# Performance work log

Measured on AMD Instinct MI355X. Metric: run time of the kernel, lower is better.

## Reference

```python
import jax, jax.numpy as jnp
import numpy as np

B = 256      # events
N_SV = 64    # secondary vertices per event
N_TRK = 512  # tracks per event
N_PFC = 512  # PF candidates per event
K = 8        # kNN neighbors
H = 32       # hidden dim


def _lin_init(key, fan_in, fan_out):
    k1, k2 = jax.random.split(key)
    lim = 1.0 / np.sqrt(fan_in)
    W = jax.random.uniform(k1, (fan_in, fan_out), minval=-lim, maxval=lim, dtype=jnp.float32)
    b = jax.random.uniform(k2, (fan_out,), minval=-lim, maxval=lim, dtype=jnp.float32)
    return W, b


def setup_inputs() -> dict:
    key = jax.random.key(0)
    ks = jax.random.split(key, 16)
    inp = {
        'x_sv': jax.random.normal(ks[0], (B * N_SV, 14), dtype=jnp.float32),
        'x_trk': jax.random.normal(ks[1], (B * N_TRK, 30), dtype=jnp.float32),
        'x_pfc': jax.random.normal(ks[2], (B * N_PFC, 10), dtype=jnp.float32),
        'batch_sv': jnp.repeat(jnp.arange(B, dtype=jnp.int64), N_SV),
        'batch_trk': jnp.repeat(jnp.arange(B, dtype=jnp.int64), N_TRK),
        'batch_pfc': jnp.repeat(jnp.arange(B, dtype=jnp.int64), N_PFC),
    }
    inp['sv_W1'], inp['sv_b1'] = _lin_init(ks[3], 14, H)
    inp['sv_W2'], inp['sv_b2'] = _lin_init(ks[4], H, H)
    inp['trk_W1'], inp['trk_b1'] = _lin_init(ks[5], 30, H)
    inp['trk_W2'], inp['trk_b2'] = _lin_init(ks[6], H, H)
    inp['pfc_W1'], inp['pfc_b1'] = _lin_init(ks[7], 10, H)
    inp['pfc_W2'], inp['pfc_b2'] = _lin_init(ks[8], H, H)
    inp['conv_W'], inp['conv_b'] = _lin_init(ks[9], 2 * H, H)  # the single shared self.conv
    inp['out_W1'], inp['out_b1'] = _lin_init(ks[10], H, H)
    inp['out_W2'], inp['out_b2'] = _lin_init(ks[11], H, 1)
    return inp


def _encode(x, W1, b1, W2, b2):
    h = jax.nn.elu(x @ W1 + b1)
    return jax.nn.elu(h @ W2 + b2)


def _edge_conv(x_src, x_dst, W, b):
    # x_src [B,Ns,H] source set, x_dst [B,Nd,H] destination/query set.
    # kNN: for each dst node, K nearest src nodes (per event) by Euclidean dist.
    d2 = (jnp.sum(x_dst * x_dst, -1)[:, :, None]
          - 2.0 * jnp.einsum('bnd,bmd->bnm', x_dst, x_src)
          + jnp.sum(x_src * x_src, -1)[:, None, :])  # [B,Nd,Ns]
    _, idx = jax.lax.top_k(-d2, K)                     # [B,Nd,K]
    x_j = jax.vmap(lambda s, i: s[i])(x_src, idx)      # [B,Nd,K,H]
    x_i = jnp.broadcast_to(x_dst[:, :, None, :], x_j.shape)
    e = jnp.concatenate([x_i, x_j - x_i], axis=-1)     # [B,Nd,K,2H]
    m = jax.nn.elu(e @ W + b)                          # edge MLP
    return jnp.max(m, axis=2)                          # max aggregation [B,Nd,H]


def reference(x_sv, x_trk, x_pfc, batch_sv, batch_trk, batch_pfc,
              sv_W1, sv_b1, sv_W2, sv_b2,
              trk_W1, trk_b1, trk_W2, trk_b2,
              pfc_W1, pfc_b1, pfc_W2, pfc_b2,
              conv_W, conv_b, out_W1, out_b1, out_W2, out_b2):
    sv = _encode(x_sv, sv_W1, sv_b1, sv_W2, sv_b2).reshape(B, N_SV, H)
    trk = _encode(x_trk, trk_W1, trk_b1, trk_W2, trk_b2).reshape(B, N_TRK, H)
    pfc = _encode(x_pfc, pfc_W1, pfc_b1, pfc_W2, pfc_b2).reshape(B, N_PFC, H)

    feats1 = _edge_conv(sv, trk, conv_W, conv_b)     # sv -> trk
    feats2 = _edge_conv(pfc, trk, conv_W, conv_b)    # pfc -> trk
    feats3 = _edge_conv(feats1, feats2, conv_W, conv_b)  # feats1 -> feats2 (both trk-sized)

    # avg_pool_x(batch_trk, feats3, batch_trk): per-event mean
    f = feats3.reshape(B * N_TRK, H)
    s = jax.ops.segment_sum(f, batch_trk, num_segments=B)
    cnt = jax.ops.segment_sum(jnp.ones((B * N_TRK,), f.dtype), batch_trk, num_segments=B)
    pooled = s / cnt[:, None]

    out = jax.nn.sigmoid(jax.nn.elu(pooled @ out_W1 + out_b1) @ out_W2 + out_b2)  # [B,1]
    return out, jnp.arange(B, dtype=jnp.int64)
```

## Files before the change

### kernel.cpp

```cpp
#include <hip/hip_runtime.h>
#include <math.h>

#define NB 256
#define KNN 8

typedef __attribute__((ext_vector_type(8))) short short8;
typedef __attribute__((ext_vector_type(4))) float f32x4;

__device__ __forceinline__ float elu_f(float x) {
    return x > 0.f ? x : __expf(x) - 1.f;
}

__device__ __forceinline__ unsigned bf16rn(float x) {
    unsigned u = __float_as_uint(x);
    return (u + 0x7FFFu + ((u >> 16) & 1u)) >> 16;
}

__device__ __forceinline__ void bfsplit(float x, short& h, short& l) {
    unsigned hu = bf16rn(x);
    h = (short)hu;
    l = (short)bf16rn(x - __uint_as_float(hu << 16));
}

__device__ __forceinline__ void cex(unsigned& a, unsigned& b) {
    unsigned lo = min(a, b), hi = max(a, b);
    a = lo; b = hi;
}

__device__ __forceinline__ void sort8(unsigned* s) {
    cex(s[0], s[1]); cex(s[2], s[3]); cex(s[4], s[5]); cex(s[6], s[7]);
    cex(s[0], s[2]); cex(s[1], s[3]); cex(s[4], s[6]); cex(s[5], s[7]);
    cex(s[1], s[2]); cex(s[5], s[6]);
    cex(s[0], s[4]); cex(s[1], s[5]); cex(s[2], s[6]); cex(s[3], s[7]);
    cex(s[2], s[4]); cex(s[3], s[5]);
    cex(s[1], s[2]); cex(s[3], s[4]); cex(s[5], s[6]);
}

__device__ __forceinline__ void merge8(unsigned* v, const unsigned* s) {
#pragma unroll
    for (int i = 0; i < 8; i++) v[i] = min(v[i], s[7 - i]);
    cex(v[0], v[4]); cex(v[1], v[5]); cex(v[2], v[6]); cex(v[3], v[7]);
    cex(v[0], v[2]); cex(v[1], v[3]); cex(v[4], v[6]); cex(v[5], v[7]);
    cex(v[0], v[1]); cex(v[2], v[3]); cex(v[4], v[5]); cex(v[6], v[7]);
}

template<int FIN, int MODE>
__device__ void encode_mfma_body(const float* __restrict__ x,
    const float* __restrict__ W1, const float* __restrict__ b1,
    const float* __restrict__ W2, const float* __restrict__ b2,
    const float* __restrict__ conv_W, const float* __restrict__ conv_b,
    float* __restrict__ enc, float* __restrict__ e1,
    unsigned short* __restrict__ hiP, unsigned short* __restrict__ loP,
    float* __restrict__ nrmP,
    int blk, float* __restrict__ sx)
{
    int tid = threadIdx.x;
    int lane = tid & 63, wv = tid >> 6;
    int c = lane & 15, kg = lane >> 4;
    size_t node0 = (size_t)blk * 256;

    {
        const float* xb = x + node0 * FIN;
        for (int i = tid; i < 8192; i += 256) {
            int n = i >> 5, f = i & 31;
            sx[i] = (f < FIN) ? xb[n * FIN + f] : 0.f;
        }
    }
    __syncthreads();

    int rb = wv * 64;

#pragma unroll
    for (int ph = 0; ph < 3; ph++) {
        short8 Bh0, Bl0, Bh1, Bl1;
#pragma unroll
        for (int e = 0; e < 8; e++) {
            int kk = kg * 8 + e;
            float w0, w1;
            if (ph == 0) {
                w0 = (kk < FIN) ? W1[kk * 32 + c] : 0.f;
                w1 = (kk < FIN) ? W1[kk * 32 + 16 + c] : 0.f;
            } else if (ph == 1) {
                w0 = W2[kk * 32 + c];
                w1 = W2[kk * 32 + 16 + c];
            } else {
                w0 = conv_W[1024 + kk * 32 + c];
                w1 = conv_W[1024 + kk * 32 + 16 + c];
                if (MODE == 1) {
                    w0 = conv_W[kk * 32 + c] - w0;
                    w1 = conv_W[kk * 32 + 16 + c] - w1;
                }
            }
            short h, l;
            bfsplit(w0, h, l); Bh0[e] = h; Bl0[e] = l;
            bfsplit(w1, h, l); Bh1[e] = h; Bl1[e] = l;
        }
        float bias0, bias1;
        if (ph == 0)      { bias0 = b1[c]; bias1 = b1[16 + c]; }
        else if (ph == 1) { bias0 = b2[c]; bias1 = b2[16 + c]; }
        else              { bias0 = (MODE == 1) ? conv_b[c] : 0.f;
                            bias1 = (MODE == 1) ? conv_b[16 + c] : 0.f; }

#pragma unroll
        for (int t = 0; t < 4; t++) {
            int tb = rb + t * 16;
            int arow = tb + c;
            const float* ap = sx + arow * 32 + kg * 8;
            float4 a0 = *(const float4*)(ap);
            float4 a1 = *(const float4*)(ap + 4);
            float av[8] = {a0.x, a0.y, a0.z, a0.w, a1.x, a1.y, a1.z, a1.w};
            short8 Ah, Al;
#pragma unroll
            for (int e = 0; e < 8; e++) {
                short h, l;
                bfsplit(av[e], h, l);
                Ah[e] = h; Al[e] = l;
            }

            if (MODE == 0 && ph == 2) {
                float nr = 0.f;
#pragma unroll
                for (int e = 0; e < 8; e++) nr = fmaf(av[e], av[e], nr);
                nr += __shfl_xor(nr, 16);
                nr += __shfl_xor(nr, 32);
                if (kg == 0) nrmP[node0 + arow] = nr;
                *(short8*)(hiP + (node0 + arow) * 32 + kg * 8) = Ah;
                *(short8*)(loP + (node0 + arow) * 32 + kg * 8) = Al;
            }

            f32x4 acc0 = {bias0, bias0, bias0, bias0};
            f32x4 acc1 = {bias1, bias1, bias1, bias1};
            acc0 = __builtin_amdgcn_mfma_f32_16x16x32_bf16(Al, Bh0, acc0, 0, 0, 0);
            acc0 = __builtin_amdgcn_mfma_f32_16x16x32_bf16(Ah, Bl0, acc0, 0, 0, 0);
            acc0 = __builtin_amdgcn_mfma_f32_16x16x32_bf16(Ah, Bh0, acc0, 0, 0, 0);
            acc1 = __builtin_amdgcn_mfma_f32_16x16x32_bf16(Al, Bh1, acc1, 0, 0, 0);
            acc1 = __builtin_amdgcn_mfma_f32_16x16x32_bf16(Ah, Bl1, acc1, 0, 0, 0);
            acc1 = __builtin_amdgcn_mfma_f32_16x16x32_bf16(Ah, Bh1, acc1, 0, 0, 0);

            int drow = tb + kg * 4;
            if (ph < 2) {
#pragma unroll
                for (int r = 0; r < 4; r++) {
                    float v0 = elu_f(acc0[r]);
                    float v1 = elu_f(acc1[r]);
                    sx[(drow + r) * 32 + c] = v0;
                    sx[(drow + r) * 32 + 16 + c] = v1;
                    if (MODE == 1 && ph == 1) {
                        size_t off = (node0 + drow + r) * 32 + c;
                        enc[off] = v0;
                        enc[off + 16] = v1;
                    }
                }
            } else {
#pragma unroll
                for (int r = 0; r < 4; r++) {
                    size_t off = (node0 + drow + r) * 32 + c;
                    e1[off] = acc0[r];
                    e1[off + 16] = acc1[r];
                }
            }
        }
    }
}

__global__ __launch_bounds__(256) void encode_all_kernel(
    const float* __restrict__ x_sv, const float* __restrict__ x_trk, const float* __restrict__ x_pfc,
    const float* __restrict__ sv_W1, const float* __restrict__ sv_b1,
    const float* __restrict__ sv_W2, const float* __restrict__ sv_b2,
    const float* __restrict__ trk_W1, const float* __restrict__ trk_b1,
    const float* __restrict__ trk_W2, const float* __restrict__ trk_b2,
    const float* __restrict__ pfc_W1, const float* __restrict__ pfc_b1,
    const float* __restrict__ pfc_W2, const float* __restrict__ pfc_b2,
    const float* __restrict__ conv_W, const float* __restrict__ conv_b,
    float* __restrict__ trk_enc,
    float* __restrict__ Y1, float* __restrict__ Y2,
    float* __restrict__ f1,
    unsigned short* __restrict__ svHi, unsigned short* __restrict__ svLo, float* __restrict__ nrm_sv,
    unsigned short* __restrict__ pfcHi, unsigned short* __restrict__ pfcLo, float* __restrict__ nrm_pfc)
{
    __shared__ float sx[8192];
    int bid = blockIdx.x;
    if (bid < 64)
        encode_mfma_body<14, 0>(x_sv, sv_W1, sv_b1, sv_W2, sv_b2, conv_W, conv_b,
                                nullptr, Y1, svHi, svLo, nrm_sv, bid, sx);
    else if (bid < 576)
        encode_mfma_body<30, 1>(x_trk, trk_W1, trk_b1, trk_W2, trk_b2, conv_W, conv_b,
                                trk_enc, f1, nullptr, nullptr, nullptr, bid - 64, sx);
    else
        encode_mfma_body<10, 0>(x_pfc, pfc_W1, pfc_b1, pfc_W2, pfc_b2, conv_W, conv_b,
                                nullptr, Y2, pfcHi, pfcLo, nrm_pfc, bid - 576, sx);
}

__device__ __forceinline__ void knn_build_B(const float* __restrict__ dstF,
                                            int dstbase, int c, int kg,
                                            short8& Bh, short8& Bl, float& nd)
{
    const float* brow = dstF + (size_t)(dstbase + c) * 32 + kg * 8;
    float4 b0 = *(const float4*)(brow);
    float4 b1 = *(const float4*)(brow + 4);
    float bx[8] = {b0.x, b0.y, b0.z, b0.w, b1.x, b1.y, b1.z, b1.w};
    nd = 0.f;
#pragma unroll
    for (int i = 0; i < 8; i++) {
        float xv = bx[i];
        nd = fmaf(xv, xv, nd);
        short h, l;
        bfsplit(xv, h, l);
        Bh[i] = h; Bl[i] = l;
    }
    nd += __shfl_xor(nd, 16);
    nd += __shfl_xor(nd, 32);
}

template<int NT>
__device__ __forceinline__ void knn_scan(
    const unsigned short* __restrict__ srcHi, const unsigned short* __restrict__ srcLo,
    const float* __restrict__ snrm,
    short8 Bh, short8 Bl, float nd, int c, int kg,
    unsigned* key)
{
    for (int t = 0; t < NT; t += 2) {
        unsigned cand[8];
#pragma unroll
        for (int u = 0; u < 2; u++) {
            int tt = t + u;
            size_t arow = ((size_t)(tt * 16 + c)) * 32 + (size_t)kg * 8;
            short8 Ah = *(const short8*)(srcHi + arow);
            short8 Al = *(const short8*)(srcLo + arow);
            f32x4 acc = {0.f, 0.f, 0.f, 0.f};
            acc = __builtin_amdgcn_mfma_f32_16x16x32_bf16(Al, Bl, acc, 0, 0, 0);
            acc = __builtin_amdgcn_mfma_f32_16x16x32_bf16(Al, Bh, acc, 0, 0, 0);
            acc = __builtin_amdgcn_mfma_f32_16x16x32_bf16(Ah, Bl, acc, 0, 0, 0);
            acc = __builtin_amdgcn_mfma_f32_16x16x32_bf16(Ah, Bh, acc, 0, 0, 0);
            float4 sn = *(const float4*)(snrm + tt * 16 + kg * 4);
            int sb = tt * 16 + kg * 4;
            cand[u*4+0] = (__float_as_uint(fmaf(-2.f, acc[0], sn.x + nd)) & 0xFFFFFE00u) | (unsigned)(sb + 0);
            cand[u*4+1] = (__float_as_uint(fmaf(-2.f, acc[1], sn.y + nd)) & 0xFFFFFE00u) | (unsigned)(sb + 1);
            cand[u*4+2] = (__float_as_uint(fmaf(-2.f, acc[2], sn.z + nd)) & 0xFFFFFE00u) | (unsigned)(sb + 2);
            cand[u*4+3] = (__float_as_uint(fmaf(-2.f, acc[3], sn.w + nd)) & 0xFFFFFE00u) | (unsigned)(sb + 3);
        }
        sort8(cand);
        merge8(key, cand);
    }
}

__device__ __forceinline__ void knn_merge_lanes(unsigned* key)
{
    unsigned oth[8];
#pragma unroll
    for (int k = 0; k < 8; k++) oth[k] = __shfl_xor(key[k], 16);
    merge8(key, oth);
#pragma unroll
    for (int k = 0; k < 8; k++) oth[k] = __shfl_xor(key[k], 32);
    merge8(key, oth);
}

__device__ __forceinline__ void gather_max8(const float* __restrict__ Yb,
                                            const unsigned* key, int kg, float* m)
{
    const float* r0 = Yb + (size_t)(key[0] & 511u) * 32 + kg * 8;
    float4 a = *(const float4*)(r0);
    float4 b = *(const float4*)(r0 + 4);
    m[0] = a.x; m[1] = a.y; m[2] = a.z; m[3] = a.w;
    m[4] = b.x; m[5] = b.y; m[6] = b.z; m[7] = b.w;
#pragma unroll
    for (int k = 1; k < 8; k++) {
        const float* rr = Yb + (size_t)(key[k] & 511u) * 32 + kg * 8;
        float4 va = *(const float4*)(rr);
        float4 vb = *(const float4*)(rr + 4);
        m[0] = fmaxf(m[0], va.x); m[1] = fmaxf(m[1], va.y);
        m[2] = fmaxf(m[2], va.z); m[3] = fmaxf(m[3], va.w);
        m[4] = fmaxf(m[4], vb.x); m[5] = fmaxf(m[5], vb.y);
        m[6] = fmaxf(m[6], vb.z); m[7] = fmaxf(m[7], vb.w);
    }
}

__global__ __launch_bounds__(256) void knn12_kernel(
    const unsigned short* __restrict__ svHi, const unsigned short* __restrict__ svLo,
    const float* __restrict__ nrm_sv,
    const unsigned short* __restrict__ pfcHi, const unsigned short* __restrict__ pfcLo,
    const float* __restrict__ nrm_pfc,
    const float* __restrict__ trk_enc,
    const float* __restrict__ Y1, const float* __restrict__ Y2,
    float* __restrict__ f1, float* __restrict__ f2,
    unsigned short* __restrict__ f1Hi, unsigned short* __restrict__ f1Lo,
    float* __restrict__ nrm_f1)
{
    int bid = blockIdx.x;
    int e = bid & 255, j = bid >> 8;
    int lane = threadIdx.x & 63, wave = threadIdx.x >> 6;
    int c = lane & 15, kg = lane >> 4;
    int dstbase = j * 64 + wave * 16;
    size_t trow = (size_t)e * 512 + dstbase + c;

    short8 Bh, Bl;
    float nd;
    knn_build_B(trk_enc + (size_t)e * 512 * 32, dstbase, c, kg, Bh, Bl, nd);

    unsigned key2[8];
#pragma unroll
    for (int k = 0; k < 8; k++) key2[k] = 0xFFFFFFFFu;
    knn_scan<32>(pfcHi + (size_t)e * 512 * 32, pfcLo + (size_t)e * 512 * 32,
                 nrm_pfc + e * 512, Bh, Bl, nd, c, kg, key2);
    knn_merge_lanes(key2);

    unsigned key1[8];
#pragma unroll
    for (int k = 0; k < 8; k++) key1[k] = 0xFFFFFFFFu;
    knn_scan<4>(svHi + (size_t)e * 64 * 32, svLo + (size_t)e * 64 * 32,
                nrm_sv + e * 64, Bh, Bl, nd, c, kg, key1);
    knn_merge_lanes(key1);

    const float* bp = f1 + trow * 32 + kg * 8;
    float4 bb0 = *(const float4*)(bp);
    float4 bb1 = *(const float4*)(bp + 4);
    float base[8] = {bb0.x, bb0.y, bb0.z, bb0.w, bb1.x, bb1.y, bb1.z, bb1.w};

    float m[8];
    gather_max8(Y2 + (size_t)e * 512 * 32, key2, kg, m);
    {
        float4 o0, o1;
        o0.x = elu_f(base[0] + m[0]); o0.y = elu_f(base[1] + m[1]);
        o0.z = elu_f(base[2] + m[2]); o0.w = elu_f(base[3] + m[3]);
        o1.x = elu_f(base[4] + m[4]); o1.y = elu_f(base[5] + m[5]);
        o1.z = elu_f(base[6] + m[6]); o1.w = elu_f(base[7] + m[7]);
        float4* op = (float4*)(f2 + trow * 32 + kg * 8);
        op[0] = o0; op[1] = o1;
    }
    gather_max8(Y1 + (size_t)e * 64 * 32, key1, kg, m);
    {
        float v[8];
        float nr = 0.f;
        short8 Hh, Hl;
#pragma unroll
        for (int i = 0; i < 8; i++) {
            v[i] = elu_f(base[i] + m[i]);
            nr = fmaf(v[i], v[i], nr);
            short h, l;
            bfsplit(v[i], h, l);
            Hh[i] = h; Hl[i] = l;
        }
        nr += __shfl_xor(nr, 16);
        nr += __shfl_xor(nr, 32);
        if (kg == 0) nrm_f1[trow] = nr;
        float4* op = (float4*)(f1 + trow * 32 + kg * 8);
        op[0] = (float4){v[0], v[1], v[2], v[3]};
        op[1] = (float4){v[4], v[5], v[6], v[7]};
        *(short8*)(f1Hi + trow * 32 + kg * 8) = Hh;
        *(short8*)(f1Lo + trow * 32 + kg * 8) = Hl;
    }
}

__global__ __launch_bounds__(256) void knn3_kernel(
    const unsigned short* __restrict__ f1Hi, const unsigned short* __restrict__ f1Lo,
    const float* __restrict__ nrm_f1,
    const float* __restrict__ f2,
    const float* __restrict__ Y3, const float* __restrict__ B3,
    float* __restrict__ pool)
{
    __shared__ float sp[4][32];
    int bid = blockIdx.x;
    int e = bid & 255, j = bid >> 8;
    int tid = threadIdx.x;
    int lane = tid & 63, wave = tid >> 6;
    int c = lane & 15, kg = lane >> 4;
    int dstbase = j * 64 + wave * 16;
    size_t trow = (size_t)e * 512 + dstbase + c;

    short8 Bh, Bl;
    float nd;
    knn_build_B(f2 + (size_t)e * 512 * 32, dstbase, c, kg, Bh, Bl, nd);

    unsigned key[8];
#pragma unroll
    for (int k = 0; k < 8; k++) key[k] = 0xFFFFFFFFu;
    knn_scan<32>(f1Hi + (size_t)e * 512 * 32, f1Lo + (size_t)e * 512 * 32,
                 nrm_f1 + e * 512, Bh, Bl, nd, c, kg, key);
    knn_merge_lanes(key);

    float m[8];
    gather_max8(Y3 + (size_t)e * 512 * 32, key, kg, m);

    const float* bp = B3 + trow * 32 + kg * 8;
    float4 bb0 = *(const float4*)(bp);
    float4 bb1 = *(const float4*)(bp + 4);
    float base[8] = {bb0.x, bb0.y, bb0.z, bb0.w, bb1.x, bb1.y, bb1.z, bb1.w};

    float r[8];
#pragma unroll
    for (int i = 0; i < 8; i++) r[i] = elu_f(base[i] + m[i]);

#pragma unroll
    for (int off = 1; off < 16; off <<= 1) {
#pragma unroll
        for (int i = 0; i < 8; i++) r[i] += __shfl_xor(r[i], off);
    }
    if (c == 0) {
#pragma unroll
        for (int i = 0; i < 8; i++) sp[wave][kg * 8 + i] = r[i];
    }
    __syncthreads();
    if (tid < 32)
        pool[((size_t)e * 8 + j) * 32 + tid] =
            sp[0][tid] + sp[1][tid] + sp[2][tid] + sp[3][tid];
}

__global__ __launch_bounds__(256) void yb3_kernel(
    const float* __restrict__ f1, const float* __restrict__ f2,
    const float* __restrict__ conv_W, const float* __restrict__ conv_b,
    float* __restrict__ Y3, float* __restrict__ B3)
{
    int bid = blockIdx.x;
    int mode = (bid >= 512);
    const float* X = mode ? f2 : f1;
    float* O = mode ? B3 : Y3;
    size_t node0 = (size_t)(mode ? bid - 512 : bid) * 256;
    int tid = threadIdx.x, lane = tid & 63, wv = tid >> 6;
    int c = lane & 15, kg = lane >> 4;

    short8 Bh0, Bl0, Bh1, Bl1;
#pragma unroll
    for (int e = 0; e < 8; e++) {
        int kk = kg * 8 + e;
        float w0 = conv_W[1024 + kk * 32 + c];
        float w1 = conv_W[1024 + kk * 32 + 16 + c];
        if (mode) {
            w0 = conv_W[kk * 32 + c] - w0;
            w1 = conv_W[kk * 32 + 16 + c] - w1;
        }
        short h, l;
        bfsplit(w0, h, l); Bh0[e] = h; Bl0[e] = l;
        bfsplit(w1, h, l); Bh1[e] = h; Bl1[e] = l;
    }
    float bias0 = mode ? conv_b[c] : 0.f;
    float bias1 = mode ? conv_b[16 + c] : 0.f;

    int rb = wv * 64;
#pragma unroll
    for (int t = 0; t < 4; t++) {
        int tb = rb + t * 16;
        int arow = tb + c;
        const float* ap = X + (node0 + arow) * 32 + kg * 8;
        float4 a0 = *(const float4*)(ap);
        float4 a1 = *(const float4*)(ap + 4);
        float av[8] = {a0.x, a0.y, a0.z, a0.w, a1.x, a1.y, a1.z, a1.w};
        short8 Ah, Al;
#pragma unroll
        for (int e = 0; e < 8; e++) {
            short h, l;
            bfsplit(av[e], h, l);
            Ah[e] = h; Al[e] = l;
        }
        f32x4 acc0 = {bias0, bias0, bias0, bias0};
        f32x4 acc1 = {bias1, bias1, bias1, bias1};
        acc0 = __builtin_amdgcn_mfma_f32_16x16x32_bf16(Al, Bh0, acc0, 0, 0, 0);
        acc0 = __builtin_amdgcn_mfma_f32_16x16x32_bf16(Ah, Bl0, acc0, 0, 0, 0);
        acc0 = __builtin_amdgcn_mfma_f32_16x16x32_bf16(Ah, Bh0, acc0, 0, 0, 0);
        acc1 = __builtin_amdgcn_mfma_f32_16x16x32_bf16(Al, Bh1, acc1, 0, 0, 0);
        acc1 = __builtin_amdgcn_mfma_f32_16x16x32_bf16(Ah, Bl1, acc1, 0, 0, 0);
        acc1 = __builtin_amdgcn_mfma_f32_16x16x32_bf16(Ah, Bh1, acc1, 0, 0, 0);

        int drow = tb + kg * 4;
#pragma unroll
        for (int r = 0; r < 4; r++) {
            size_t off = (node0 + drow + r) * 32 + c;
            O[off] = acc0[r];
            O[off + 16] = acc1[r];
        }
    }
}

__global__ __launch_bounds__(64) void final_kernel(
    const float* __restrict__ pool,
    const float* __restrict__ W1, const float* __restrict__ b1,
    const float* __restrict__ W2, const float* __restrict__ b2,
    float* __restrict__ outp)
{
    int b = blockIdx.x;
    int lane = threadIdx.x, c = lane & 31;
    __shared__ float sp[32];
    __shared__ float sh1[32];
    if (lane < 32) {
        float s = 0.f;
#pragma unroll
        for (int jj = 0; jj < 8; jj++)
            s += pool[((size_t)b * 8 + jj) * 32 + c];
        sp[c] = s * (1.0f / 512.0f);
    }
    __syncthreads();
    if (lane < 32) {
        float h = b1[c];
#pragma unroll
        for (int d = 0; d < 32; d++) h = fmaf(sp[d], W1[d * 32 + c], h);
        sh1[c] = elu_f(h);
    }
    __syncthreads();
    if (lane == 0) {
        float o = b2[0];
#pragma unroll
        for (int d = 0; d < 32; d++) o = fmaf(sh1[d], W2[d], o);
        o = 1.f / (1.f + __expf(-o));
        outp[b] = o;
        outp[NB + b] = (float)b;
    }
}

extern "C" void kernel_launch(void* const* d_in, const int* in_sizes, int n_in,
                              void* d_out, int out_size, void* d_ws, size_t ws_size,
                              hipStream_t stream) {
    const float* x_sv  = (const float*)d_in[0];
    const float* x_trk = (const float*)d_in[1];
    const float* x_pfc = (const float*)d_in[2];
    const float* sv_W1  = (const float*)d_in[6];
    const float* sv_b1  = (const float*)d_in[7];
    const float* sv_W2  = (const float*)d_in[8];
    const float* sv_b2  = (const float*)d_in[9];
    const float* trk_W1 = (const float*)d_in[10];
    const float* trk_b1 = (const float*)d_in[11];
    const float* trk_W2 = (const float*)d_in[12];
    const float* trk_b2 = (const float*)d_in[13];
    const float* pfc_W1 = (const float*)d_in[14];
    const float* pfc_b1 = (const float*)d_in[15];
    const float* pfc_W2 = (const float*)d_in[16];
    const float* pfc_b2 = (const float*)d_in[17];
    const float* conv_W = (const float*)d_in[18];
    const float* conv_b = (const float*)d_in[19];
    const float* out_W1 = (const float*)d_in[20];
    const float* out_b1 = (const float*)d_in[21];
    const float* out_W2 = (const float*)d_in[22];
    const float* out_b2 = (const float*)d_in[23];

    float* ws = (float*)d_ws;
    const size_t SV_E  = (size_t)NB * 64 * 32;
    const size_t TRK_E = (size_t)NB * 512 * 32;
    float* f1      = ws;
    float* f2      = f1 + TRK_E;
    float* trk_enc = f2 + TRK_E;
    float* Y1      = trk_enc + TRK_E;
    float* Y2      = Y1 + SV_E;
    unsigned short* svHi  = (unsigned short*)(Y2 + TRK_E);
    unsigned short* svLo  = svHi + SV_E;
    unsigned short* pfcHi = svLo + SV_E;
    unsigned short* pfcLo = pfcHi + TRK_E;
    unsigned short* f1Hi  = pfcLo + TRK_E;
    unsigned short* f1Lo  = f1Hi + TRK_E;
    float* nrm_sv  = (float*)(f1Lo + TRK_E);
    float* nrm_pfc = nrm_sv + (size_t)NB * 64;
    float* nrm_f1  = nrm_pfc + (size_t)NB * 512;
    float* Y3   = trk_enc;
    float* B3   = (float*)pfcHi;
    float* pool = (float*)svHi;

    encode_all_kernel<<<1088, 256, 0, stream>>>(
        x_sv, x_trk, x_pfc,
        sv_W1, sv_b1, sv_W2, sv_b2,
        trk_W1, trk_b1, trk_W2, trk_b2,
        pfc_W1, pfc_b1, pfc_W2, pfc_b2,
        conv_W, conv_b,
        trk_enc, Y1, Y2, f1,
        svHi, svLo, nrm_sv, pfcHi, pfcLo, nrm_pfc);

    knn12_kernel<<<2048, 256, 0, stream>>>(svHi, svLo, nrm_sv,
                                           pfcHi, pfcLo, nrm_pfc,
                                           trk_enc, Y1, Y2,
                                           f1, f2, f1Hi, f1Lo, nrm_f1);

    yb3_kernel<<<1024, 256, 0, stream>>>(f1, f2, conv_W, conv_b, Y3, B3);
    knn3_kernel<<<2048, 256, 0, stream>>>(f1Hi, f1Lo, nrm_f1, f2, Y3, B3, pool);

    final_kernel<<<NB, 64, 0, stream>>>(pool, out_W1, out_b1, out_W2, out_b2, (float*)d_out);
}
```

Baseline: 303.9 us.

## Fuse Y3/B3 conv projections into knn12 kernel, dropping yb3 kernel

The knn12 kernel now computes the edge-conv linear projections (Y3 from f1, B3 from f2 with the bias and the W difference) right after producing f1/f2, using split-bf16 MFMA in registers. This removes the separate yb3 kernel launch, the fp32 f1 store, and the reload of f1 and f2 from global memory. B3 now aliases the f1base buffer and Y3 aliases trk_enc. Each wave only overwrites rows it has already read, so the aliasing is safe. In exchange, knn12 carries more registers for the weight fragments, which may reduce occupancy.

```diff
diff --git a/kernel.cpp b/kernel.cpp
--- a/kernel.cpp
+++ b/kernel.cpp
@@ -174,7 +174,7 @@
     const float* __restrict__ conv_W, const float* __restrict__ conv_b,
     float* __restrict__ trk_enc,
     float* __restrict__ Y1, float* __restrict__ Y2,
-    float* __restrict__ f1,
+    float* __restrict__ f1base,
     unsigned short* __restrict__ svHi, unsigned short* __restrict__ svLo, float* __restrict__ nrm_sv,
     unsigned short* __restrict__ pfcHi, unsigned short* __restrict__ pfcLo, float* __restrict__ nrm_pfc)
 {
@@ -185,7 +185,7 @@
                                 nullptr, Y1, svHi, svLo, nrm_sv, bid, sx);
     else if (bid < 576)
         encode_mfma_body<30, 1>(x_trk, trk_W1, trk_b1, trk_W2, trk_b2, conv_W, conv_b,
-                                trk_enc, f1, nullptr, nullptr, nullptr, bid - 64, sx);
+                                trk_enc, f1base, nullptr, nullptr, nullptr, bid - 64, sx);
     else
         encode_mfma_body<10, 0>(x_pfc, pfc_W1, pfc_b1, pfc_W2, pfc_b2, conv_W, conv_b,
                                 nullptr, Y2, pfcHi, pfcLo, nrm_pfc, bid - 576, sx);
@@ -282,16 +282,35 @@
     const float* __restrict__ nrm_pfc,
     const float* __restrict__ trk_enc,
     const float* __restrict__ Y1, const float* __restrict__ Y2,
-    float* __restrict__ f1, float* __restrict__ f2,
+    const float* __restrict__ f1base, float* __restrict__ f2,
     unsigned short* __restrict__ f1Hi, unsigned short* __restrict__ f1Lo,
-    float* __restrict__ nrm_f1)
+    float* __restrict__ nrm_f1,
+    float* __restrict__ Y3, float* __restrict__ B3,
+    const float* __restrict__ conv_W, const float* __restrict__ conv_b)
 {
     int bid = blockIdx.x;
     int e = bid & 255, j = bid >> 8;
-    int lane = threadIdx.x & 63, wave = threadIdx.x >> 6;
+    int tid = threadIdx.x;
+    int lane = tid & 63, wave = tid >> 6;
     int c = lane & 15, kg = lane >> 4;
     int dstbase = j * 64 + wave * 16;
     size_t trow = (size_t)e * 512 + dstbase + c;
+
+    short8 WYh0, WYl0, WYh1, WYl1, WDh0, WDl0, WDh1, WDl1;
+#pragma unroll
+    for (int ee = 0; ee < 8; ee++) {
+        int kk = kg * 8 + ee;
+        float y0 = conv_W[1024 + kk * 32 + c];
+        float y1 = conv_W[1024 + kk * 32 + 16 + c];
+        float d0 = conv_W[kk * 32 + c] - y0;
+        float d1 = conv_W[kk * 32 + 16 + c] - y1;
+        short h, l;
+        bfsplit(y0, h, l); WYh0[ee] = h; WYl0[ee] = l;
+        bfsplit(y1, h, l); WYh1[ee] = h; WYl1[ee] = l;
+        bfsplit(d0, h, l); WDh0[ee] = h; WDl0[ee] = l;
+        bfsplit(d1, h, l); WDh1[ee] = h; WDl1[ee] = l;
+    }
+    float bd0 = conv_b[c], bd1 = conv_b[16 + c];
 
     short8 Bh, Bl;
     float nd;
@@ -311,43 +330,67 @@
                 nrm_sv + e * 64, Bh, Bl, nd, c, kg, key1);
     knn_merge_lanes(key1);
 
-    const float* bp = f1 + trow * 32 + kg * 8;
+    const float* bp = f1base + trow * 32 + kg * 8;
     float4 bb0 = *(const float4*)(bp);
     float4 bb1 = *(const float4*)(bp + 4);
     float base[8] = {bb0.x, bb0.y, bb0.z, bb0.w, bb1.x, bb1.y, bb1.z, bb1.w};
 
     float m[8];
     gather_max8(Y2 + (size_t)e * 512 * 32, key2, kg, m);
+    float v2[8];
+    short8 Fh, Fl;
+#pragma unroll
+    for (int i = 0; i < 8; i++) {
+        v2[i] = elu_f(base[i] + m[i]);
+        short h, l;
+        bfsplit(v2[i], h, l);
+        Fh[i] = h; Fl[i] = l;
+    }
     {
-        float4 o0, o1;
-        o0.x = elu_f(base[0] + m[0]); o0.y = elu_f(base[1] + m[1]);
-        o0.z = elu_f(base[2] + m[2]); o0.w = elu_f(base[3] + m[3]);
-        o1.x = elu_f(base[4] + m[4]); o1.y = elu_f(base[5] + m[5]);
-        o1.z = elu_f(base[6] + m[6]); o1.w = elu_f(base[7] + m[7]);
         float4* op = (float4*)(f2 + trow * 32 + kg * 8);
-        op[0] = o0; op[1] = o1;
-    }
+        op[0] = (float4){v2[0], v2[1], v2[2], v2[3]};
+        op[1] = (float4){v2[4], v2[5], v2[6], v2[7]};
+    }
+
     gather_max8(Y1 + (size_t)e * 64 * 32, key1, kg, m);
-    {
-        float v[8];
-        float nr = 0.f;
-        short8 Hh, Hl;
-#pragma unroll
-        for (int i = 0; i < 8; i++) {
-            v[i] = elu_f(base[i] + m[i]);
-            nr = fmaf(v[i], v[i], nr);
-            short h, l;
-            bfsplit(v[i], h, l);
-            Hh[i] = h; Hl[i] = l;
-        }
-        nr += __shfl_xor(nr, 16);
-        nr += __shfl_xor(nr, 32);
-        if (kg == 0) nrm_f1[trow] = nr;
-        float4* op = (float4*)(f1 + trow * 32 + kg * 8);
-        op[0] = (float4){v[0], v[1], v[2], v[3]};
-        op[1] = (float4){v[4], v[5], v[6], v[7]};
-        *(short8*)(f1Hi + trow * 32 + kg * 8) = Hh;
-        *(short8*)(f1Lo + trow * 32 + kg * 8) = Hl;
+    float v1[8];
+    float nr = 0.f;
+    short8 Hh, Hl;
+#pragma unroll
+    for (int i = 0; i < 8; i++) {
+        v1[i] = elu_f(base[i] + m[i]);
+        nr = fmaf(v1[i], v1[i], nr);
+        short h, l;
+        bfsplit(v1[i], h, l);
+        Hh[i] = h; Hl[i] = l;
+    }
+    nr += __shfl_xor(nr, 16);
+    nr += __shfl_xor(nr, 32);
+    if (kg == 0) nrm_f1[trow] = nr;
+    *(short8*)(f1Hi + trow * 32 + kg * 8) = Hh;
+    *(short8*)(f1Lo + trow * 32 + kg * 8) = Hl;
+
+    f32x4 a0 = {0.f, 0.f, 0.f, 0.f}, a1 = {0.f, 0.f, 0.f, 0.f};
+    a0 = __builtin_amdgcn_mfma_f32_16x16x32_bf16(Hl, WYh0, a0, 0, 0, 0);
+    a0 = __builtin_amdgcn_mfma_f32_16x16x32_bf16(Hh, WYl0, a0, 0, 0, 0);
+    a0 = __builtin_amdgcn_mfma_f32_16x16x32_bf16(Hh, WYh0, a0, 0, 0, 0);
+    a1 = __builtin_amdgcn_mfma_f32_16x16x32_bf16(Hl, WYh1, a1, 0, 0, 0);
+    a1 = __builtin_amdgcn_mfma_f32_16x16x32_bf16(Hh, WYl1, a1, 0, 0, 0);
+    a1 = __builtin_amdgcn_mfma_f32_16x16x32_bf16(Hh, WYh1, a1, 0, 0, 0);
+    f32x4 q0 = {bd0, bd0, bd0, bd0}, q1 = {bd1, bd1, bd1, bd1};
+    q0 = __builtin_amdgcn_mfma_f32_16x16x32_bf16(Fl, WDh0, q0, 0, 0, 0);
+    q0 = __builtin_amdgcn_mfma_f32_16x16x32_bf16(Fh, WDl0, q0, 0, 0, 0);
+    q0 = __builtin_amdgcn_mfma_f32_16x16x32_bf16(Fh, WDh0, q0, 0, 0, 0);
+    q1 = __builtin_amdgcn_mfma_f32_16x16x32_bf16(Fl, WDh1, q1, 0, 0, 0);
+    q1 = __builtin_amdgcn_mfma_f32_16x16x32_bf16(Fh, WDl1, q1, 0, 0, 0);
+    q1 = __builtin_amdgcn_mfma_f32_16x16x32_bf16(Fh, WDh1, q1, 0, 0, 0);
+
+    int drow = dstbase + kg * 4;
+#pragma unroll
+    for (int r = 0; r < 4; r++) {
+        size_t off = ((size_t)e * 512 + drow + r) * 32 + c;
+        Y3[off] = a0[r];  Y3[off + 16] = a1[r];
+        B3[off] = q0[r];  B3[off + 16] = q1[r];
     }
 }
 
@@ -403,71 +446,6 @@
     if (tid < 32)
         pool[((size_t)e * 8 + j) * 32 + tid] =
             sp[0][tid] + sp[1][tid] + sp[2][tid] + sp[3][tid];
-}
-
-__global__ __launch_bounds__(256) void yb3_kernel(
-    const float* __restrict__ f1, const float* __restrict__ f2,
-    const float* __restrict__ conv_W, const float* __restrict__ conv_b,
-    float* __restrict__ Y3, float* __restrict__ B3)
-{
-    int bid = blockIdx.x;
-    int mode = (bid >= 512);
-    const float* X = mode ? f2 : f1;
-    float* O = mode ? B3 : Y3;
-    size_t node0 = (size_t)(mode ? bid - 512 : bid) * 256;
-    int tid = threadIdx.x, lane = tid & 63, wv = tid >> 6;
-    int c = lane & 15, kg = lane >> 4;
-
-    short8 Bh0, Bl0, Bh1, Bl1;
-#pragma unroll
-    for (int e = 0; e < 8; e++) {
-        int kk = kg * 8 + e;
-        float w0 = conv_W[1024 + kk * 32 + c];
-        float w1 = conv_W[1024 + kk * 32 + 16 + c];
-        if (mode) {
-            w0 = conv_W[kk * 32 + c] - w0;
-            w1 = conv_W[kk * 32 + 16 + c] - w1;
-        }
-        short h, l;
-        bfsplit(w0, h, l); Bh0[e] = h; Bl0[e] = l;
-        bfsplit(w1, h, l); Bh1[e] = h; Bl1[e] = l;
-    }
-    float bias0 = mode ? conv_b[c] : 0.f;
-    float bias1 = mode ? conv_b[16 + c] : 0.f;
-
-    int rb = wv * 64;
-#pragma unroll
-    for (int t = 0; t < 4; t++) {
-        int tb = rb + t * 16;
-        int arow = tb + c;
-        const float* ap = X + (node0 + arow) * 32 + kg * 8;
-        float4 a0 = *(const float4*)(ap);
-        float4 a1 = *(const float4*)(ap + 4);
-        float av[8] = {a0.x, a0.y, a0.z, a0.w, a1.x, a1.y, a1.z, a1.w};
-        short8 Ah, Al;
-#pragma unroll
-        for (int e = 0; e < 8; e++) {
-            short h, l;
-            bfsplit(av[e], h, l);
-            Ah[e] = h; Al[e] = l;
-        }
-        f32x4 acc0 = {bias0, bias0, bias0, bias0};
-        f32x4 acc1 = {bias1, bias1, bias1, bias1};
-        acc0 = __builtin_amdgcn_mfma_f32_16x16x32_bf16(Al, Bh0, acc0, 0, 0, 0);
-        acc0 = __builtin_amdgcn_mfma_f32_16x16x32_bf16(Ah, Bl0, acc0, 0, 0, 0);
-        acc0 = __builtin_amdgcn_mfma_f32_16x16x32_bf16(Ah, Bh0, acc0, 0, 0, 0);
-        acc1 = __builtin_amdgcn_mfma_f32_16x16x32_bf16(Al, Bh1, acc1, 0, 0, 0);
-        acc1 = __builtin_amdgcn_mfma_f32_16x16x32_bf16(Ah, Bl1, acc1, 0, 0, 0);
-        acc1 = __builtin_amdgcn_mfma_f32_16x16x32_bf16(Ah, Bh1, acc1, 0, 0, 0);
-
-        int drow = tb + kg * 4;
-#pragma unroll
-        for (int r = 0; r < 4; r++) {
-            size_t off = (node0 + drow + r) * 32 + c;
-            O[off] = acc0[r];
-            O[off + 16] = acc1[r];
-        }
-    }
 }
 
 __global__ __launch_bounds__(64) void final_kernel(
@@ -533,8 +511,8 @@
     float* ws = (float*)d_ws;
     const size_t SV_E  = (size_t)NB * 64 * 32;
     const size_t TRK_E = (size_t)NB * 512 * 32;
-    float* f1      = ws;
-    float* f2      = f1 + TRK_E;
+    float* f1base  = ws;
+    float* f2      = f1base + TRK_E;
     float* trk_enc = f2 + TRK_E;
     float* Y1      = trk_enc + TRK_E;
     float* Y2      = Y1 + SV_E;
@@ -548,7 +526,7 @@
     float* nrm_pfc = nrm_sv + (size_t)NB * 64;
     float* nrm_f1  = nrm_pfc + (size_t)NB * 512;
     float* Y3   = trk_enc;
-    float* B3   = (float*)pfcHi;
+    float* B3   = f1base;
     float* pool = (float*)svHi;
 
     encode_all_kernel<<<1088, 256, 0, stream>>>(
@@ -557,15 +535,15 @@
         trk_W1, trk_b1, trk_W2, trk_b2,
         pfc_W1, pfc_b1, pfc_W2, pfc_b2,
         conv_W, conv_b,
-        trk_enc, Y1, Y2, f1,
+        trk_enc, Y1, Y2, f1base,
         svHi, svLo, nrm_sv, pfcHi, pfcLo, nrm_pfc);
 
     knn12_kernel<<<2048, 256, 0, stream>>>(svHi, svLo, nrm_sv,
                                            pfcHi, pfcLo, nrm_pfc,
                                            trk_enc, Y1, Y2,
-                                           f1, f2, f1Hi, f1Lo, nrm_f1);
-
-    yb3_kernel<<<1024, 256, 0, stream>>>(f1, f2, conv_W, conv_b, Y3, B3);
+                                           f1base, f2, f1Hi, f1Lo, nrm_f1,
+                                           Y3, B3, conv_W, conv_b);
+
     knn3_kernel<<<2048, 256, 0, stream>>>(f1Hi, f1Lo, nrm_f1, f2, Y3, B3, pool);
 
     final_kernel<<<NB, 64, 0, stream>>>(pool, out_W1, out_b1, out_W2, out_b2, (float*)d_out);
```

Result: faster. 295.8 us (-2.7%).
